# Performance work log

Hardware: AMD Instinct MI355X
Metric: run time of the kernel (lower is better)

## Reference

```python
import jax, jax.numpy as jnp
import numpy as np

N_NODES = 50000
N_EDGES = 800000
D_IN, D_HID, D_OUT = 64, 64, 1


def gcn_layer(x, src, dst, W, b):
    """GCN conv: linear transform, then degree-normalized scatter-add over edges
    (with self-loops), matching x' = D^-1/2 (A+I) D^-1/2 X W^T + b."""
    n = x.shape[0]
    h = x @ W.T + b                                   # [N, out]
    deg = jax.ops.segment_sum(jnp.ones_like(dst, dtype=h.dtype), dst,
                              num_segments=n) + 1.0   # +1 for self-loop
    inv_sqrt_deg = jax.lax.rsqrt(deg)                 # [N]
    coef = inv_sqrt_deg[src] * inv_sqrt_deg[dst]      # [E]
    msgs = h[src] * coef[:, None]                     # gather + scale
    agg = jax.ops.segment_sum(msgs, dst, num_segments=n)   # scatter-add
    agg = agg + h * (inv_sqrt_deg * inv_sqrt_deg)[:, None]  # self-loop term
    return agg


def setup_inputs() -> dict:
    key = jax.random.key(0)
    k = jax.random.split(key, 9)
    x = jax.random.normal(k[0], (N_NODES, D_IN), dtype=jnp.float32)
    edge_index = jax.random.randint(k[1], (2, N_EDGES), 0, N_NODES, dtype=jnp.int64)
    s = 0.1
    W0 = jax.random.normal(k[2], (D_HID, D_IN), dtype=jnp.float32) * s
    b0 = jnp.zeros((D_HID,), dtype=jnp.float32)
    W1 = jax.random.normal(k[3], (D_HID, D_HID), dtype=jnp.float32) * s
    b1 = jnp.zeros((D_HID,), dtype=jnp.float32)
    W2 = jax.random.normal(k[4], (D_OUT, D_HID), dtype=jnp.float32) * s
    b2 = jnp.zeros((D_OUT,), dtype=jnp.float32)
    return {"x": x, "edge_index": edge_index,
            "W0": W0, "b0": b0, "W1": W1, "b1": b1, "W2": W2, "b2": b2}


def reference(x, edge_index, W0, b0, W1, b1, W2, b2):
    src, dst = edge_index[0], edge_index[1]
    h = jax.nn.relu(gcn_layer(x, src, dst, W0, b0))
    h = jax.nn.relu(gcn_layer(h, src, dst, W1, b1))
    out = gcn_layer(h, src, dst, W2, b2)   # [N, 1] per-node logits
    return out
```

## Files before the change

kernel.cpp:

```cpp
#include <hip/hip_runtime.h>

#define N_NODES 50000
#define N_EDGES 800000
#define DMAX 64
#define ZROW N_NODES
#define NB 196
#define CELL 40
#define P1_BLKS 512
#define LIN_BLKS 3125
#define CH (50001 * 32)
#define GSUB 1563
typedef unsigned short u16;

__device__ __forceinline__ u16 f2bf(float f) {
    unsigned u = __builtin_bit_cast(unsigned, f);
    u += 0x7FFFu + ((u >> 16) & 1u);
    return (u16)(u >> 16);
}
__device__ __forceinline__ float bflo(unsigned u) {
    return __builtin_bit_cast(float, u << 16);
}
__device__ __forceinline__ float bfhi(unsigned u) {
    return __builtin_bit_cast(float, u & 0xFFFF0000u);
}

__global__ __launch_bounds__(256) void bin_lin0_k(
    const int* __restrict__ src, const int* __restrict__ dst,
    unsigned* __restrict__ payload, unsigned char* __restrict__ counts,
    const float* __restrict__ x, const float* __restrict__ W,
    const float* __restrict__ b, u16* __restrict__ hA)
{
    __shared__ float4 smem4[2009];
    int bid = blockIdx.x;
    int tid = threadIdx.x;
    if (bid < P1_BLKS) {
        unsigned* cur = (unsigned*)smem4;
        unsigned* pay = cur + NB;
        for (int i = tid; i < NB; i += 256) cur[i] = 0;
        __syncthreads();
        const int4* dst4 = (const int4*)dst;
        const int4* src4 = (const int4*)src;
        const int NQ = N_EDGES / 4;
        for (int q = bid * 256 + tid; q < NQ; q += P1_BLKS * 256) {
            int4 d = dst4[q];
            int4 s = src4[q];
#define BIN(dd, ss)                                                        \
            {                                                              \
                int bkt = (dd) >> 8;                                       \
                unsigned v = ((unsigned)(ss) << 8) | ((unsigned)(dd) & 255u); \
                int p = atomicAdd((int*)&cur[bkt], 1);                     \
                if (p < CELL) pay[bkt * CELL + p] = v;                     \
            }
            BIN(d.x, s.x) BIN(d.y, s.y) BIN(d.z, s.z) BIN(d.w, s.w)
#undef BIN
        }
        __syncthreads();
        unsigned* pg = payload + (size_t)bid * (NB * CELL);
        for (int i = tid; i < NB * CELL; i += 256) pg[i] = pay[i];
        for (int i = tid; i < NB; i += 256)
            counts[bid * NB + i] = (unsigned char)min((int)cur[i], CELL);
    } else {
        float* Ws = (float*)smem4;
        float* xs = (float*)smem4 + 64 * 68;
        int j = tid & 63, ln = tid >> 6;
        int nb = (bid - P1_BLKS) * 16;
        const float4* W4 = (const float4*)W;
#pragma unroll
        for (int i = 0; i < 4; ++i) {
            int idx4 = i * 256 + tid;
            *(float4*)&Ws[(idx4 >> 4) * 68 + (idx4 & 15) * 4] = W4[idx4];
        }
        {
            const float4* x4 = (const float4*)(x + (size_t)nb * 64);
            float4 v = x4[tid];
            *(float4*)&xs[(tid >> 4) * 68 + (tid & 15) * 4] = v;
        }
        __syncthreads();
        float a0 = b[j], a1 = a0, a2 = a0, a3 = a0;
        const float4* wp = (const float4*)&Ws[j * 68];
        const float4* p0 = (const float4*)&xs[(ln * 4 + 0) * 68];
        const float4* p1 = (const float4*)&xs[(ln * 4 + 1) * 68];
        const float4* p2 = (const float4*)&xs[(ln * 4 + 2) * 68];
        const float4* p3 = (const float4*)&xs[(ln * 4 + 3) * 68];
#pragma unroll
        for (int k4 = 0; k4 < 16; ++k4) {
            float4 w = wp[k4];
            float4 q0 = p0[k4]; a0 += w.x*q0.x + w.y*q0.y + w.z*q0.z + w.w*q0.w;
            float4 q1 = p1[k4]; a1 += w.x*q1.x + w.y*q1.y + w.z*q1.z + w.w*q1.w;
            float4 q2 = p2[k4]; a2 += w.x*q2.x + w.y*q2.y + w.z*q2.z + w.w*q2.w;
            float4 q3 = p3[k4]; a3 += w.x*q3.x + w.y*q3.y + w.z*q3.z + w.w*q3.w;
        }
        size_t cbase = (size_t)(j >> 5) * CH + (j & 31);
        hA[cbase + (size_t)(nb + ln * 4 + 0) * 32] = f2bf(a0);
        hA[cbase + (size_t)(nb + ln * 4 + 1) * 32] = f2bf(a1);
        hA[cbase + (size_t)(nb + ln * 4 + 2) * 32] = f2bf(a2);
        hA[cbase + (size_t)(nb + ln * 4 + 3) * 32] = f2bf(a3);
    }
}

__global__ __launch_bounds__(256) void place_k(
    const unsigned* __restrict__ payload, const unsigned char* __restrict__ counts,
    int* __restrict__ cnt, u16* __restrict__ csr,
    u16* __restrict__ hA, u16* __restrict__ hB)
{
    __shared__ int cur[256];
    int b = blockIdx.x, tid = threadIdx.x;
    cur[tid] = 0;
    __syncthreads();
    int base = b << 8;
    for (int sb = tid; sb < P1_BLKS; sb += 256) {
        int c = counts[sb * NB + b];
        const unsigned* cell = payload + ((size_t)sb * NB + b) * CELL;
        for (int k = 0; k < c; ++k) {
            unsigned v = cell[k];
            int loc = (int)(v & 255u);
            int slot = atomicAdd(&cur[loc], 1);
            if (slot < DMAX) csr[(size_t)(base + loc) * 64 + slot] = (u16)(v >> 8);
        }
    }
    __syncthreads();
    int n = base + tid;
    if (n < N_NODES) {
        int c = cur[tid];
        cnt[n] = c;
        int m = min(c, DMAX);
        for (int k = m; k < DMAX; ++k) csr[(size_t)n * 64 + k] = (u16)ZROW;
        float inv = rsqrtf((float)c + 1.f);
#pragma unroll
        for (int ch = 0; ch < 2; ++ch) {
            unsigned* row = (unsigned*)&hA[(size_t)ch * CH + (size_t)n * 32];
#pragma unroll
            for (int i2 = 0; i2 < 16; ++i2) {
                unsigned u = row[i2];
                float lo = bflo(u) * inv, hi = bfhi(u) * inv;
                row[i2] = ((unsigned)f2bf(hi) << 16) | f2bf(lo);
            }
        }
    }
    if (b == 0 && tid < 64) {
        int ch = tid >> 5, pos = tid & 31;
        hA[(size_t)ch * CH + (size_t)ZROW * 32 + pos] = 0;
        hB[(size_t)ch * CH + (size_t)ZROW * 32 + pos] = 0;
        csr[(size_t)ZROW * 64 + tid] = (u16)ZROW;
        if (tid == 0) cnt[ZROW] = 0;
    }
}

__device__ __forceinline__ float4 cgather(
    const u16* __restrict__ hc, const int* __restrict__ cnt,
    const u16* __restrict__ csr, u16* lds_w ,
    int nq, int lane, int oct, int r, float& invn_out, int& nmy_out)
{
#pragma unroll
    for (int i = 0; i < 4; ++i) {
        int u = i * 64 + lane;
        int row = u >> 5, col = u & 31;
        int nn = nq + row;
        nn = nn < N_NODES ? nn : ZROW;
        *(unsigned*)&lds_w[row * 68 + col * 2] = ((const unsigned*)csr)[nn * 32 + col];
    }
    int nmy = nq + oct;
    nmy_out = nmy;
    int nuse = nmy < N_NODES ? nmy : ZROW;
    int mc = cnt[nuse];
    float invn = rsqrtf((float)mc + 1.f);
    invn_out = invn;
    int m8 = (min(mc, DMAX) + 7) & ~7;
    int kmax = m8;
    kmax = max(kmax, __shfl_xor(kmax, 8, 64));
    kmax = max(kmax, __shfl_xor(kmax, 16, 64));
    kmax = max(kmax, __shfl_xor(kmax, 32, 64));
    __builtin_amdgcn_wave_barrier();
    const uint2* hp = (const uint2*)hc;
    uint2 sv = hp[(unsigned)(nuse * 8 + r)];
    float a0 = bflo(sv.x), a1 = bfhi(sv.x), a2 = bflo(sv.y), a3 = bfhi(sv.y);
    const u16* myrow = lds_w + oct * 68;
#pragma unroll 1
    for (int k = 0; k < kmax; k += 8) {
#pragma unroll
        for (int u = 0; u < 8; ++u) {
            int s = (int)myrow[k + u];
            uint2 v = hp[(unsigned)(s * 8 + r)];
            a0 += bflo(v.x); a1 += bfhi(v.x);
            a2 += bflo(v.y); a3 += bfhi(v.y);
        }
    }
    float4 o; o.x = a0; o.y = a1; o.z = a2; o.w = a3;
    return o;
}

__global__ __launch_bounds__(256) void gath1_k(const u16* __restrict__ hA,
                                               const int* __restrict__ cnt,
                                               const u16* __restrict__ csr,
                                               u16* __restrict__ rs) {
    __shared__ u16 cs[4][8][68];
    int tid = threadIdx.x, lane = tid & 63, w = tid >> 6;
    int oct = (tid >> 3) & 7, r = tid & 7;
    int set = blockIdx.x & 1, sub = blockIdx.x >> 1;
    int nq = sub * 32 + w * 8;
    const u16* hc = hA + (size_t)set * CH;
    float invn; int nmy;
    float4 a = cgather(hc, cnt, csr, &cs[w][0][0], nq, lane, oct, r, invn, nmy);
    if (nmy < N_NODES) {
        float f0 = fmaxf(a.x * invn, 0.f), f1 = fmaxf(a.y * invn, 0.f);
        float f2 = fmaxf(a.z * invn, 0.f), f3 = fmaxf(a.w * invn, 0.f);
        uint2 o;
        o.x = ((unsigned)f2bf(f1) << 16) | f2bf(f0);
        o.y = ((unsigned)f2bf(f3) << 16) | f2bf(f2);
        ((uint2*)(rs + (size_t)set * CH))[(unsigned)(nmy * 8 + r)] = o;
    }
}

__global__ __launch_bounds__(256) void mv1_k(const u16* __restrict__ rs,
                                             const int* __restrict__ cnt,
                                             const float* __restrict__ W,
                                             const float* __restrict__ b,
                                             u16* __restrict__ hB) {
    __shared__ float Ws[64 * 68];
    __shared__ float xs[16 * 68];
    int tid = threadIdx.x, j = tid & 63, ln = tid >> 6;
    int nb = blockIdx.x * 16;
    const float4* W4 = (const float4*)W;
#pragma unroll
    for (int i = 0; i < 4; ++i) {
        int idx4 = i * 256 + tid;
        *(float4*)&Ws[(idx4 >> 4) * 68 + (idx4 & 15) * 4] = W4[idx4];
    }
    {
        int t = tid >> 4, r16 = tid & 15;
        int c = r16 >> 3, g = r16 & 7;
        int n = nb + t;
        uint2 u = ((const uint2*)(rs + (size_t)c * CH))[(unsigned)(n * 8 + g)];
        float* xp = &xs[t * 68 + c * 32 + g * 4];
        xp[0] = bflo(u.x); xp[1] = bfhi(u.x);
        xp[2] = bflo(u.y); xp[3] = bfhi(u.y);
    }
    __syncthreads();
    float a0 = b[j], a1 = a0, a2 = a0, a3 = a0;
    const float4* wp = (const float4*)&Ws[j * 68];
    const float4* p0 = (const float4*)&xs[(ln * 4 + 0) * 68];
    const float4* p1 = (const float4*)&xs[(ln * 4 + 1) * 68];
    const float4* p2 = (const float4*)&xs[(ln * 4 + 2) * 68];
    const float4* p3 = (const float4*)&xs[(ln * 4 + 3) * 68];
#pragma unroll
    for (int k4 = 0; k4 < 16; ++k4) {
        float4 w = wp[k4];
        float4 q0 = p0[k4]; a0 += w.x*q0.x + w.y*q0.y + w.z*q0.z + w.w*q0.w;
        float4 q1 = p1[k4]; a1 += w.x*q1.x + w.y*q1.y + w.z*q1.z + w.w*q1.w;
        float4 q2 = p2[k4]; a2 += w.x*q2.x + w.y*q2.y + w.z*q2.z + w.w*q2.w;
        float4 q3 = p3[k4]; a3 += w.x*q3.x + w.y*q3.y + w.z*q3.z + w.w*q3.w;
    }
    size_t cbase = (size_t)(j >> 5) * CH + (j & 31);
    int n0 = nb + ln * 4;
    float i0 = rsqrtf((float)cnt[n0 + 0] + 1.f);
    float i1 = rsqrtf((float)cnt[n0 + 1] + 1.f);
    float i2 = rsqrtf((float)cnt[n0 + 2] + 1.f);
    float i3 = rsqrtf((float)cnt[n0 + 3] + 1.f);
    hB[cbase + (size_t)(n0 + 0) * 32] = f2bf(a0 * i0);
    hB[cbase + (size_t)(n0 + 1) * 32] = f2bf(a1 * i1);
    hB[cbase + (size_t)(n0 + 2) * 32] = f2bf(a2 * i2);
    hB[cbase + (size_t)(n0 + 3) * 32] = f2bf(a3 * i3);
}

__global__ __launch_bounds__(256) void gath2_k(const u16* __restrict__ hB,
                                               const int* __restrict__ cnt,
                                               const u16* __restrict__ csr,
                                               const float* __restrict__ W2,
                                               float* __restrict__ pd) {
    __shared__ u16 cs[4][8][68];
    int tid = threadIdx.x, lane = tid & 63, w = tid >> 6;
    int oct = (tid >> 3) & 7, r = tid & 7;
    int set = blockIdx.x & 1, sub = blockIdx.x >> 1;
    int nq = sub * 32 + w * 8;
    const u16* hc = hB + (size_t)set * CH;
    float invn; int nmy;
    float4 a = cgather(hc, cnt, csr, &cs[w][0][0], nq, lane, oct, r, invn, nmy);
    const float4 wv = ((const float4*)W2)[set * 8 + r];
    float p = fmaxf(a.x * invn, 0.f) * wv.x + fmaxf(a.y * invn, 0.f) * wv.y
            + fmaxf(a.z * invn, 0.f) * wv.z + fmaxf(a.w * invn, 0.f) * wv.w;
    p += __shfl_xor(p, 1, 64);
    p += __shfl_xor(p, 2, 64);
    p += __shfl_xor(p, 4, 64);
    if (r == 0 && nmy < N_NODES) pd[(size_t)set * N_NODES + nmy] = p;
}

__global__ __launch_bounds__(256) void comb_k(const float* __restrict__ pd,
                                              const int* __restrict__ cnt,
                                              const float* __restrict__ b2,
                                              float* __restrict__ h2) {
    int n = blockIdx.x * 256 + threadIdx.x;
    if (n < N_NODES) {
        float s = pd[n] + pd[N_NODES + n];
        h2[n] = (s + b2[0]) * rsqrtf((float)cnt[n] + 1.f);
    }
}

__global__ __launch_bounds__(256) void g1_k(const float* __restrict__ h2,
                                            const int* __restrict__ cnt,
                                            const u16* __restrict__ csr,
                                            float* __restrict__ out) {
    int tid = threadIdx.x, j = tid & 63, w = tid >> 6;
    int nb = blockIdx.x * 16;
#pragma unroll 1
    for (int t = 0; t < 4; ++t) {
        int n = nb + w * 4 + t;
        int mf = cnt[n];
        int m = min(mf, DMAX);
        float invn = rsqrtf((float)mf + 1.f);
        float v = 0.f;
        if (j < m) v = h2[(int)csr[(size_t)n * 64 + j]];
#pragma unroll
        for (int off = 32; off; off >>= 1) v += __shfl_xor(v, off, 64);
        if (j == 0) out[n] = (v + h2[n]) * invn;
    }
}

extern "C" void kernel_launch(void* const* d_in, const int* in_sizes, int n_in,
                              void* d_out, int out_size, void* d_ws, size_t ws_size,
                              hipStream_t stream) {
    const float* x  = (const float*)d_in[0];
    const int*   ei = (const int*)d_in[1];
    const float* W0 = (const float*)d_in[2];
    const float* b0 = (const float*)d_in[3];
    const float* W1 = (const float*)d_in[4];
    const float* b1 = (const float*)d_in[5];
    const float* W2 = (const float*)d_in[6];
    const float* b2 = (const float*)d_in[7];
    float* out = (float*)d_out;

    char* ws = (char*)d_ws;
    size_t off = 0;
    auto alloc = [&](size_t bytes) {
        void* p = ws + off;
        off = (off + bytes + 255) & ~(size_t)255;
        return p;
    };
    int*      cnt  = (int*)alloc((size_t)(N_NODES + 1) * 4);
    u16*      csr  = (u16*)alloc((size_t)(N_NODES + 1) * DMAX * 2);
    u16*      hA   = (u16*)alloc((size_t)2 * CH * 2);
    u16*      hB   = (u16*)alloc((size_t)2 * CH * 2);
    u16*      rs   = (u16*)alloc((size_t)2 * CH * 2);
    float*    pd   = (float*)alloc((size_t)2 * N_NODES * 4);
    float*    h2   = (float*)alloc((size_t)N_NODES * 4);
    unsigned* payload = (unsigned*)alloc((size_t)P1_BLKS * NB * CELL * 4);
    unsigned char* counts = (unsigned char*)alloc((size_t)P1_BLKS * NB);

    const int* src = ei;
    const int* dst = ei + N_EDGES;

    bin_lin0_k<<<P1_BLKS + LIN_BLKS, 256, 0, stream>>>(src, dst, payload, counts,
                                                       x, W0, b0, hA);
    place_k<<<NB, 256, 0, stream>>>(payload, counts, cnt, csr, hA, hB);
    gath1_k<<<GSUB * 2, 256, 0, stream>>>(hA, cnt, csr, rs);
    mv1_k<<<LIN_BLKS, 256, 0, stream>>>(rs, cnt, W1, b1, hB);
    gath2_k<<<GSUB * 2, 256, 0, stream>>>(hB, cnt, csr, W2, pd);
    comb_k<<<196, 256, 0, stream>>>(pd, cnt, b2, h2);
    g1_k<<<LIN_BLKS, 256, 0, stream>>>(h2, cnt, csr, out);
}
```

Measured before the change: 94.74 us.

## Compact binning payload, split prescale kernel, widen gather unroll, fuse final combine

The binning blocks now run a prefix scan over per-bucket counts and write a compacted payload with per-cell offsets, so less data is written and read. The node prescale by inverse sqrt degree moves out of the 196-block place kernel into a separate fully parallel kernel. The gather inner loop is unrolled by 16 instead of 8, and comb_k is fused into the final gather, which now recomputes h2 on the fly. Cell capacity drops from 40 to 32, which raises the chance of silently dropping edges in crowded buckets; the fused final kernel also repeats per-neighbor rsqrt and pd loads.

```diff
diff --git a/kernel.cpp b/kernel.cpp
--- a/kernel.cpp
+++ b/kernel.cpp
@@ -5,8 +5,9 @@
 #define DMAX 64
 #define ZROW N_NODES
 #define NB 196
-#define CELL 40
+#define CELL 32
 #define P1_BLKS 512
+#define BLK_EDGE_CAP 2048
 #define LIN_BLKS 3125
 #define CH (50001 * 32)
 #define GSUB 1563
@@ -27,15 +28,17 @@
 __global__ __launch_bounds__(256) void bin_lin0_k(
     const int* __restrict__ src, const int* __restrict__ dst,
     unsigned* __restrict__ payload, unsigned char* __restrict__ counts,
+    u16* __restrict__ offs,
     const float* __restrict__ x, const float* __restrict__ W,
     const float* __restrict__ b, u16* __restrict__ hA)
 {
-    __shared__ float4 smem4[2009];
+    __shared__ unsigned smem[6664];
     int bid = blockIdx.x;
     int tid = threadIdx.x;
     if (bid < P1_BLKS) {
-        unsigned* cur = (unsigned*)smem4;
-        unsigned* pay = cur + NB;
+        unsigned* cur  = smem;
+        unsigned* base = smem + NB;
+        unsigned* pay  = smem + 2 * NB;
         for (int i = tid; i < NB; i += 256) cur[i] = 0;
         __syncthreads();
         const int4* dst4 = (const int4*)dst;
@@ -55,13 +58,30 @@
 #undef BIN
         }
         __syncthreads();
-        unsigned* pg = payload + (size_t)bid * (NB * CELL);
-        for (int i = tid; i < NB * CELL; i += 256) pg[i] = pay[i];
-        for (int i = tid; i < NB; i += 256)
-            counts[bid * NB + i] = (unsigned char)min((int)cur[i], CELL);
+        if (tid < NB) base[tid] = min(cur[tid], (unsigned)CELL);
+        __syncthreads();
+        for (int d = 1; d < NB; d <<= 1) {
+            unsigned v = 0;
+            if (tid < NB && tid >= d) v = base[tid - d];
+            __syncthreads();
+            if (tid < NB) base[tid] += v;
+            __syncthreads();
+        }
+        if (tid < NB) {
+            unsigned c = min(cur[tid], (unsigned)CELL);
+            counts[bid * NB + tid] = (unsigned char)c;
+            offs[bid * NB + tid]   = (u16)(base[tid] - c);
+        }
+        __syncthreads();
+        unsigned* pg = payload + (size_t)bid * BLK_EDGE_CAP;
+        for (int idx = tid; idx < NB * CELL; idx += 256) {
+            int i = idx >> 5, k = idx & 31;
+            unsigned c = min(cur[i], (unsigned)CELL);
+            if ((unsigned)k < c) pg[base[i] - c + k] = pay[idx];
+        }
     } else {
-        float* Ws = (float*)smem4;
-        float* xs = (float*)smem4 + 64 * 68;
+        float* Ws = (float*)smem;
+        float* xs = (float*)smem + 64 * 68;
         int j = tid & 63, ln = tid >> 6;
         int nb = (bid - P1_BLKS) * 16;
         const float4* W4 = (const float4*)W;
@@ -100,6 +120,7 @@
 
 __global__ __launch_bounds__(256) void place_k(
     const unsigned* __restrict__ payload, const unsigned char* __restrict__ counts,
+    const u16* __restrict__ offs,
     int* __restrict__ cnt, u16* __restrict__ csr,
     u16* __restrict__ hA, u16* __restrict__ hB)
 {
@@ -110,7 +131,7 @@
     int base = b << 8;
     for (int sb = tid; sb < P1_BLKS; sb += 256) {
         int c = counts[sb * NB + b];
-        const unsigned* cell = payload + ((size_t)sb * NB + b) * CELL;
+        const unsigned* cell = payload + (size_t)sb * BLK_EDGE_CAP + offs[sb * NB + b];
         for (int k = 0; k < c; ++k) {
             unsigned v = cell[k];
             int loc = (int)(v & 255u);
@@ -125,17 +146,6 @@
         cnt[n] = c;
         int m = min(c, DMAX);
         for (int k = m; k < DMAX; ++k) csr[(size_t)n * 64 + k] = (u16)ZROW;
-        float inv = rsqrtf((float)c + 1.f);
-#pragma unroll
-        for (int ch = 0; ch < 2; ++ch) {
-            unsigned* row = (unsigned*)&hA[(size_t)ch * CH + (size_t)n * 32];
-#pragma unroll
-            for (int i2 = 0; i2 < 16; ++i2) {
-                unsigned u = row[i2];
-                float lo = bflo(u) * inv, hi = bfhi(u) * inv;
-                row[i2] = ((unsigned)f2bf(hi) << 16) | f2bf(lo);
-            }
-        }
     }
     if (b == 0 && tid < 64) {
         int ch = tid >> 5, pos = tid & 31;
@@ -146,6 +156,26 @@
     }
 }
 
+__global__ __launch_bounds__(256) void presc_k(const int* __restrict__ cnt,
+                                               u16* __restrict__ hA) {
+    int gid = blockIdx.x * 256 + threadIdx.x;
+    int n = gid >> 3, g = gid & 7;
+    if (n >= N_NODES) return;
+    float inv = rsqrtf((float)cnt[n] + 1.f);
+    uint2* h0 = (uint2*)hA;
+    uint2* h1 = (uint2*)(hA + (size_t)CH);
+#pragma unroll
+    for (int c = 0; c < 2; ++c) {
+        uint2* hp = c ? h1 : h0;
+        uint2 u = hp[(unsigned)(n * 8 + g)];
+        float l0 = bflo(u.x) * inv, h0v = bfhi(u.x) * inv;
+        float l1 = bflo(u.y) * inv, h1v = bfhi(u.y) * inv;
+        u.x = ((unsigned)f2bf(h0v) << 16) | f2bf(l0);
+        u.y = ((unsigned)f2bf(h1v) << 16) | f2bf(l1);
+        hp[(unsigned)(n * 8 + g)] = u;
+    }
+}
+
 __device__ __forceinline__ float4 cgather(
     const u16* __restrict__ hc, const int* __restrict__ cnt,
     const u16* __restrict__ csr, u16* lds_w ,
@@ -165,8 +195,8 @@
     int mc = cnt[nuse];
     float invn = rsqrtf((float)mc + 1.f);
     invn_out = invn;
-    int m8 = (min(mc, DMAX) + 7) & ~7;
-    int kmax = m8;
+    int m16 = (min(mc, DMAX) + 15) & ~15;
+    int kmax = m16;
     kmax = max(kmax, __shfl_xor(kmax, 8, 64));
     kmax = max(kmax, __shfl_xor(kmax, 16, 64));
     kmax = max(kmax, __shfl_xor(kmax, 32, 64));
@@ -176,9 +206,9 @@
     float a0 = bflo(sv.x), a1 = bfhi(sv.x), a2 = bflo(sv.y), a3 = bfhi(sv.y);
     const u16* myrow = lds_w + oct * 68;
 #pragma unroll 1
-    for (int k = 0; k < kmax; k += 8) {
-#pragma unroll
-        for (int u = 0; u < 8; ++u) {
+    for (int k = 0; k < kmax; k += 16) {
+#pragma unroll
+        for (int u = 0; u < 16; ++u) {
             int s = (int)myrow[k + u];
             uint2 v = hp[(unsigned)(s * 8 + r)];
             a0 += bflo(v.x); a1 += bfhi(v.x);
@@ -284,23 +314,14 @@
     if (r == 0 && nmy < N_NODES) pd[(size_t)set * N_NODES + nmy] = p;
 }
 
-__global__ __launch_bounds__(256) void comb_k(const float* __restrict__ pd,
-                                              const int* __restrict__ cnt,
-                                              const float* __restrict__ b2,
-                                              float* __restrict__ h2) {
-    int n = blockIdx.x * 256 + threadIdx.x;
-    if (n < N_NODES) {
-        float s = pd[n] + pd[N_NODES + n];
-        h2[n] = (s + b2[0]) * rsqrtf((float)cnt[n] + 1.f);
-    }
-}
-
-__global__ __launch_bounds__(256) void g1_k(const float* __restrict__ h2,
-                                            const int* __restrict__ cnt,
-                                            const u16* __restrict__ csr,
-                                            float* __restrict__ out) {
+__global__ __launch_bounds__(256) void g1c_k(const float* __restrict__ pd,
+                                             const int* __restrict__ cnt,
+                                             const u16* __restrict__ csr,
+                                             const float* __restrict__ b2,
+                                             float* __restrict__ out) {
     int tid = threadIdx.x, j = tid & 63, w = tid >> 6;
     int nb = blockIdx.x * 16;
+    float b2s = b2[0];
 #pragma unroll 1
     for (int t = 0; t < 4; ++t) {
         int n = nb + w * 4 + t;
@@ -308,10 +329,16 @@
         int m = min(mf, DMAX);
         float invn = rsqrtf((float)mf + 1.f);
         float v = 0.f;
-        if (j < m) v = h2[(int)csr[(size_t)n * 64 + j]];
+        if (j < m) {
+            int s = (int)csr[(size_t)n * 64 + j];
+            v = (pd[s] + pd[N_NODES + s] + b2s) * rsqrtf((float)cnt[s] + 1.f);
+        }
 #pragma unroll
         for (int off = 32; off; off >>= 1) v += __shfl_xor(v, off, 64);
-        if (j == 0) out[n] = (v + h2[n]) * invn;
+        if (j == 0) {
+            float h2n = (pd[n] + pd[N_NODES + n] + b2s) * invn;
+            out[n] = (v + h2n) * invn;
+        }
     }
 }
 
@@ -341,19 +368,19 @@
     u16*      hB   = (u16*)alloc((size_t)2 * CH * 2);
     u16*      rs   = (u16*)alloc((size_t)2 * CH * 2);
     float*    pd   = (float*)alloc((size_t)2 * N_NODES * 4);
-    float*    h2   = (float*)alloc((size_t)N_NODES * 4);
-    unsigned* payload = (unsigned*)alloc((size_t)P1_BLKS * NB * CELL * 4);
+    unsigned* payload = (unsigned*)alloc((size_t)P1_BLKS * BLK_EDGE_CAP * 4);
     unsigned char* counts = (unsigned char*)alloc((size_t)P1_BLKS * NB);
+    u16*      offs = (u16*)alloc((size_t)P1_BLKS * NB * 2);
 
     const int* src = ei;
     const int* dst = ei + N_EDGES;
 
     bin_lin0_k<<<P1_BLKS + LIN_BLKS, 256, 0, stream>>>(src, dst, payload, counts,
-                                                       x, W0, b0, hA);
-    place_k<<<NB, 256, 0, stream>>>(payload, counts, cnt, csr, hA, hB);
+                                                       offs, x, W0, b0, hA);
+    place_k<<<NB, 256, 0, stream>>>(payload, counts, offs, cnt, csr, hA, hB);
+    presc_k<<<1563, 256, 0, stream>>>(cnt, hA);
     gath1_k<<<GSUB * 2, 256, 0, stream>>>(hA, cnt, csr, rs);
     mv1_k<<<LIN_BLKS, 256, 0, stream>>>(rs, cnt, W1, b1, hB);
     gath2_k<<<GSUB * 2, 256, 0, stream>>>(hB, cnt, csr, W2, pd);
-    comb_k<<<196, 256, 0, stream>>>(pd, cnt, b2, h2);
-    g1_k<<<LIN_BLKS, 256, 0, stream>>>(h2, cnt, csr, out);
-}
+    g1c_k<<<LIN_BLKS, 256, 0, stream>>>(pd, cnt, csr, b2, out);
+}
```

Result: slower. 105.2 us (+11.0%).
